# Kernel optimization log

Measured on AMD Instinct MI355X. Metric: run time of the kernel, lower is better.

## Reference

```python
import jax, jax.numpy as jnp
import numpy as np

RES = 0.1
TABLE = 1 << 20  # hash_table_size, power of two
PRIMES = np.array([73856093, 19349669, 83492791], dtype=np.int64)
FEAT_DIM = 120
BMIN = (-2.6, -8.1, 0.0)
BMAX = (4.6, 4.7, 3.1)
M_QUERIES = 1_000_000
CORNERS = np.array([[0,0,0],[1,0,0],[0,1,0],[0,0,1],[1,1,0],[1,0,1],[0,1,1],[1,1,1]], dtype=np.int32)


def _build_table():
    # Replicates build_hash_grid(): first-come voxel index per hash slot, collisions skipped.
    xs = np.arange(BMIN[0], BMAX[0], RES, dtype=np.float32)
    ys = np.arange(BMIN[1], BMAX[1], RES, dtype=np.float32)
    zs = np.arange(BMIN[2], BMAX[2], RES, dtype=np.float32)
    gx, gy, gz = np.meshgrid(xs, ys, zs, indexing='ij')
    coords = np.stack([gx, gy, gz], -1).reshape(-1, 3)
    gc = np.floor(coords / RES).astype(np.int64)
    h = np.remainder((gc * PRIMES).sum(-1), TABLE)
    n = coords.shape[0]
    buf = np.full(TABLE, -1, dtype=np.int32)
    buf[h[::-1]] = np.arange(n, dtype=np.int32)[::-1]
    return buf, n


def setup_inputs() -> dict:
    key = jax.random.key(0)
    k1, k2 = jax.random.split(key)
    buf, n_vox = _build_table()
    lo = jnp.array(BMIN, jnp.float32)
    hi = jnp.array(BMAX, jnp.float32)
    query_pts = lo + (hi - lo) * jax.random.uniform(k1, (M_QUERIES, 3), dtype=jnp.float32)
    features = 0.01 * jax.random.normal(k2, (n_vox, FEAT_DIM), dtype=jnp.float32)
    return {
        "query_pts": query_pts,
        "features": features,
        "buffer_voxel_index": jnp.asarray(buf),  # int32 [TABLE]
    }


def reference(query_pts, features, buffer_voxel_index):
    """query_voxel_feature with trilinear_feat=True: 8-corner hash lookup + trilinear blend."""
    primes_u = jnp.asarray(PRIMES.astype(np.uint32))
    gcf = query_pts / RES                        # [M,3]
    floor = jnp.floor(gcf)
    frac = gcf - floor                           # [M,3]
    base = floor.astype(jnp.int32)               # [M,3]
    acc = jnp.zeros((query_pts.shape[0], features.shape[1]), dtype=features.dtype)
    for c in CORNERS:                            # fixed 8-iteration corner loop
        cj = jnp.asarray(c)
        cc = base + cj                           # [M,3]
        # TABLE is a power of two, so low-20-bits of wrapping uint32 arithmetic
        # equals the exact int64 remainder used by torch.
        h = ((cc.astype(jnp.uint32) * primes_u).sum(-1) & (TABLE - 1)).astype(jnp.int32)
        vidx = buffer_voxel_index[h]             # [M], -1 for empty slots
        w = jnp.where(cj == 0, 1.0 - frac, frac).prod(-1)  # [M] trilinear weight
        w = jnp.where(vidx >= 0, w, 0.0)
        acc = acc + features[jnp.maximum(vidx, 0)] * w[:, None]
    return acc
```

## Files before the change

### kernel.cpp

```cpp
#include <hip/hip_runtime.h>


#define TABLE_MASK ((1u << 20) - 1u)
#define FEAT_DIM 120
#define ROW_STRIDE 120
#define NROWS 75
#define NCHUNK 30
#define TOTCH (NROWS * NCHUNK)
#define NSLOT 5
#define NXCD 8
#define C8 32

#define NBINS_X 32
#define NBINS_Y 64
#define NBINS_Z 16
#define NBINS (NBINS_X * NBINS_Y * NBINS_Z)

typedef float f4 __attribute__((ext_vector_type(4)));

__global__ __launch_bounds__(256) void zero_kernel(int* __restrict__ hist8) {
    const int i = blockIdx.x * blockDim.x + threadIdx.x;
    if (i < NXCD * NBINS + 2) hist8[i] = 0;
}

__global__ __launch_bounds__(256) void bin_kernel(
    const float* __restrict__ qp, int* __restrict__ hist8,
    f4* __restrict__ sq8, f4* __restrict__ ovf, int Cr, int M)
{
    const int q = blockIdx.x * blockDim.x + threadIdx.x;
    if (q >= M) return;

    int xcd;
    asm volatile("s_getreg_b32 %0, hwreg(HW_REG_XCC_ID)" : "=s"(xcd));
    xcd &= (NXCD - 1);

    const float gx = qp[3 * q + 0] / 0.1f;
    const float gy = qp[3 * q + 1] / 0.1f;
    const float gz = qp[3 * q + 2] / 0.1f;
    const int bx = (int)floorf(gx);
    const int by = (int)floorf(gy);
    const int bz = (int)floorf(gz);
    const int kx = ((bx + 32) >> 2) & (NBINS_X - 1);
    const int ky = ((by + 96) >> 2) & (NBINS_Y - 1);
    const int kz = (bz >> 1) & (NBINS_Z - 1);
    const int key = ((kx * NBINS_Y) + ky) * NBINS_Z + kz;

    const int pos = __hip_atomic_fetch_add(&hist8[xcd * NBINS + key], 1,
                                           __ATOMIC_RELAXED,
                                           __HIP_MEMORY_SCOPE_WORKGROUP);
    f4 s;
    s.x = gx; s.y = gy; s.z = gz; s.w = __int_as_float(q);
    if (pos < Cr) {
        sq8[((size_t)xcd * NBINS + key) * C8 + pos] = s;
    } else {
        const int o = atomicAdd(&hist8[NXCD * NBINS], 1);
        if (o < M) ovf[o] = s;
    }
}

__global__ __launch_bounds__(256) void compact_kernel(
    const int* __restrict__ hist8, int* __restrict__ nact,
    int* __restrict__ list)
{
    const int i = blockIdx.x * blockDim.x + threadIdx.x;
    if (i >= NBINS) return;
    int tot = 0;
#pragma unroll
    for (int s = 0; s < NXCD; ++s) tot += hist8[s * NBINS + i];
    if (tot > 0) {
        const int p = atomicAdd(nact, 1);
        list[p] = i;
    }
}

__global__ __launch_bounds__(512, 4) void voxel_trilinear_kernel(
    const f4*    __restrict__ sq8,
    const float* __restrict__ feat,
    const int*   __restrict__ table,
    const int*   __restrict__ hist8,
    const int*   __restrict__ nactp,
    const int*   __restrict__ list,
    float*       __restrict__ out,
    int Cr)
{
    __shared__ f4    sqL[NXCD * C8];
    __shared__ float rows[NROWS * ROW_STRIDE];

    const int t = threadIdx.x;
    const int nact = *nactp;
    const int stride = gridDim.x;

    if (blockIdx.x >= nact) return;

    f4   rreg[NSLOT];
    f4   qreg;
    bool qok = false;
    int  qdst = 0;
    int  total = 0;

    auto prefetch = [&](int wg) {
        int c[8];
#pragma unroll
        for (int i = 0; i < 8; ++i) {
            int v = hist8[i * NBINS + wg];
            c[i] = (v > Cr) ? Cr : v;
        }
        total = 0;
#pragma unroll
        for (int i = 0; i < 8; ++i) total += c[i];

        qok = false;
        if (t < 256) {
            const int seg = t >> 5, lane = t & 31;
            int p = 0;
#pragma unroll
            for (int i = 0; i < 8; ++i) p += (i < seg) ? c[i] : 0;
            if (lane < c[seg]) {
                qok = true;
                qdst = p + lane;
                qreg = sq8[((size_t)seg * NBINS + wg) * C8 + lane];
            }
        }

        const int binx = wg >> 10;
        const int biny = (wg >> 4) & 63;
        const int binz = wg & 15;
        const int vx0 = binx * 4 - 32;
        const int vy0 = biny * 4 - 96;
        const int vz0 = binz * 2;
#pragma unroll
        for (int s = 0; s < NSLOT; ++s) {
            const int idx = t + s * 512;
            f4 val = (f4)(0.0f);
            if (idx < TOTCH) {
                const int row = idx / NCHUNK;
                const int chunk = idx - row * NCHUNK;
                const int i = row / 15;
                const int j = (row / 3) % 5;
                const int k = row % 3;
                const unsigned h = (unsigned)(vx0 + i) * 73856093u
                                 + (unsigned)(vy0 + j) * 19349669u
                                 + (unsigned)(vz0 + k) * 83492791u;
                const int v = table[h & TABLE_MASK];
                if (v >= 0)
                    val = *reinterpret_cast<const f4*>(
                        feat + (size_t)v * FEAT_DIM + chunk * 4);
            }
            rreg[s] = val;
        }
    };

    prefetch(list[blockIdx.x]);

    for (int bi = blockIdx.x; bi < nact; bi += stride) {
        __syncthreads();

#pragma unroll
        for (int s = 0; s < NSLOT; ++s) {
            const int idx = t + s * 512;
            if (idx < TOTCH)
                *reinterpret_cast<f4*>(rows + idx * 4) = rreg[s];
        }
        if (qok) sqL[qdst] = qreg;
        const int ct = total;
        __syncthreads();

        const int nb = bi + stride;
        if (nb < nact) prefetch(list[nb]);

        const int group = t >> 4;
        const int l = t & 15;
        const int CX[8] = {0, 1, 0, 0, 1, 1, 0, 1};
        const int CY[8] = {0, 0, 1, 0, 1, 0, 1, 1};
        const int CZ[8] = {0, 0, 0, 1, 0, 1, 1, 1};

        for (int qs = group; qs < ct; qs += 32) {
            const f4 qv = sqL[qs];
            const float rx = qv.x - floorf(qv.x);
            const float ry = qv.y - floorf(qv.y);
            const float rz = qv.z - floorf(qv.z);
            const int q = __float_as_int(qv.w);
            const int lx = ((int)floorf(qv.x) + 32) & 3;
            const int ly = ((int)floorf(qv.y) + 96) & 3;
            const int lz = (int)floorf(qv.z) & 1;

            const float sx = 1.0f - rx, sy = 1.0f - ry, sz = 1.0f - rz;
            float w[8];
            w[0] = sx * sy * sz;
            w[1] = rx * sy * sz;
            w[2] = sx * ry * sz;
            w[3] = sx * sy * rz;
            w[4] = rx * ry * sz;
            w[5] = rx * sy * rz;
            w[6] = sx * ry * rz;
            w[7] = rx * ry * rz;

            f4 a0 = (f4)(0.0f), a1 = (f4)(0.0f);
#pragma unroll
            for (int k = 0; k < 8; ++k) {
                const int row = ((lx + CX[k]) * 5 + (ly + CY[k])) * 3 + (lz + CZ[k]);
                const float* rp = rows + row * ROW_STRIDE;
                const f4 fa = *reinterpret_cast<const f4*>(rp + l * 4);
                const f4 fb = *reinterpret_cast<const f4*>(rp + 56 + l * 4);
                a0 += fa * w[k];
                a1 += fb * w[k];
            }

            float* po = out + (size_t)q * FEAT_DIM;
            __builtin_nontemporal_store(a0, reinterpret_cast<f4*>(po + l * 4));
            if (l >= 2)
                __builtin_nontemporal_store(a1, reinterpret_cast<f4*>(po + 56 + l * 4));
        }
    }
}

__global__ __launch_bounds__(256) void ovf_kernel(
    const f4*    __restrict__ ovf,
    const int*   __restrict__ hist8,
    const float* __restrict__ feat,
    const int*   __restrict__ table,
    float*       __restrict__ out,
    int M)
{
    int n = hist8[NXCD * NBINS];
    if (n > M) n = M;
    if (n == 0) return;

    const int nthreads = gridDim.x * 256;
    for (int i = blockIdx.x * 256 + threadIdx.x; i < n * 16; i += nthreads) {
        const int g = i >> 4;
        const int l = i & 15;
        const f4 qv = ovf[g];
        const float gx = qv.x, gy = qv.y, gz = qv.z;
        const int q = __float_as_int(qv.w);
        const float flx = floorf(gx), fly = floorf(gy), flz = floorf(gz);
        const float rx = gx - flx, ry = gy - fly, rz = gz - flz;
        const int bx = (int)flx, by = (int)fly, bz = (int)flz;

        const unsigned hx0 = (unsigned)bx * 73856093u;
        const unsigned hy0 = (unsigned)by * 19349669u;
        const unsigned hz0 = (unsigned)bz * 83492791u;
        const unsigned hx1 = hx0 + 73856093u;
        const unsigned hy1 = hy0 + 19349669u;
        const unsigned hz1 = hz0 + 83492791u;

        unsigned h[8];
        h[0] = (hx0 + hy0 + hz0) & TABLE_MASK;
        h[1] = (hx1 + hy0 + hz0) & TABLE_MASK;
        h[2] = (hx0 + hy1 + hz0) & TABLE_MASK;
        h[3] = (hx0 + hy0 + hz1) & TABLE_MASK;
        h[4] = (hx1 + hy1 + hz0) & TABLE_MASK;
        h[5] = (hx1 + hy0 + hz1) & TABLE_MASK;
        h[6] = (hx0 + hy1 + hz1) & TABLE_MASK;
        h[7] = (hx1 + hy1 + hz1) & TABLE_MASK;

        int vidx[8];
#pragma unroll
        for (int k = 0; k < 8; ++k) vidx[k] = table[h[k]];

        const float sxw = 1.0f - rx, syw = 1.0f - ry, szw = 1.0f - rz;
        float w[8];
        w[0] = sxw * syw * szw;
        w[1] = rx  * syw * szw;
        w[2] = sxw * ry  * szw;
        w[3] = sxw * syw * rz;
        w[4] = rx  * ry  * szw;
        w[5] = rx  * syw * rz;
        w[6] = sxw * ry  * rz;
        w[7] = rx  * ry  * rz;

        f4 a0 = (f4)(0.0f), a1 = (f4)(0.0f);
#pragma unroll
        for (int k = 0; k < 8; ++k) {
            const int v = vidx[k] >= 0 ? vidx[k] : 0;
            const float wk = vidx[k] >= 0 ? w[k] : 0.0f;
            const float* rp = feat + (size_t)v * FEAT_DIM;
            const f4 fa = *reinterpret_cast<const f4*>(rp + l * 4);
            const f4 fb = *reinterpret_cast<const f4*>(rp + 56 + l * 4);
            a0 += fa * wk;
            a1 += fb * wk;
        }

        float* po = out + (size_t)q * FEAT_DIM;
        __builtin_nontemporal_store(a0, reinterpret_cast<f4*>(po + l * 4));
        if (l >= 2)
            __builtin_nontemporal_store(a1, reinterpret_cast<f4*>(po + 56 + l * 4));
    }
}

extern "C" void kernel_launch(void* const* d_in, const int* in_sizes, int n_in,
                              void* d_out, int out_size, void* d_ws, size_t ws_size,
                              hipStream_t stream) {
    const float* qp    = (const float*)d_in[0];
    const float* feat  = (const float*)d_in[1];
    const int*   table = (const int*)d_in[2];
    float*       out   = (float*)d_out;

    const int M = in_sizes[0] / 3;

    const size_t histB = ((NXCD * NBINS + 2) * sizeof(int) + 15) & ~(size_t)15;
    const size_t listB = (NBINS * sizeof(int) + 15) & ~(size_t)15;
    int* hist8 = (int*)d_ws;
    int* nact  = hist8 + NXCD * NBINS + 1;
    int* list  = (int*)((char*)d_ws + histB);
    f4*  ovf   = (f4*)((char*)d_ws + histB + listB);
    f4*  sq8   = ovf + M;

    const size_t fixed = histB + listB + (size_t)M * 16;
    size_t cap = (ws_size > fixed)
               ? (ws_size - fixed) / ((size_t)NXCD * NBINS * 16) : 0;
    int Cr = (cap > C8) ? C8 : (int)cap;
    if (Cr < 1) Cr = 1;

    const int block = 256;
    zero_kernel<<<(NXCD * NBINS + 2 + block - 1) / block, block, 0, stream>>>(hist8);
    bin_kernel<<<(M + block - 1) / block, block, 0, stream>>>(qp, hist8, sq8, ovf, Cr, M);
    compact_kernel<<<(NBINS + block - 1) / block, block, 0, stream>>>(hist8, nact, list);
    voxel_trilinear_kernel<<<1024, 512, 0, stream>>>(sq8, feat, table, hist8,
                                                     nact, list, out, Cr);
    ovf_kernel<<<512, 256, 0, stream>>>(ovf, hist8, feat, table, out, M);
}
```

Baseline: 234.5 us.

## Order bins big-first and shrink per-XCD slot capacity to twelve

Compaction now splits active bins into a big list (at least 40 points) filled from the front and a small list filled from the back, so the persistent voxel kernel processes heavy bins first and light edge bins last. The per-XCD slot capacity per bin is reduced from 32 to 12, shrinking the staging buffer and the threads used to load queries into shared memory. Points beyond the capacity spill to the slower overflow kernel, so more queries may take the global per-point path.

```diff
diff --git a/kernel.cpp b/kernel.cpp
--- a/kernel.cpp
+++ b/kernel.cpp
@@ -9,7 +9,8 @@
 #define TOTCH (NROWS * NCHUNK)
 #define NSLOT 5
 #define NXCD 8
-#define C8 32
+#define C8 12
+#define BIGTHR 40
 
 #define NBINS_X 32
 #define NBINS_Y 64
@@ -20,7 +21,7 @@
 
 __global__ __launch_bounds__(256) void zero_kernel(int* __restrict__ hist8) {
     const int i = blockIdx.x * blockDim.x + threadIdx.x;
-    if (i < NXCD * NBINS + 2) hist8[i] = 0;
+    if (i < NXCD * NBINS + 3) hist8[i] = 0;
 }
 
 __global__ __launch_bounds__(256) void bin_kernel(
@@ -59,17 +60,18 @@
 }
 
 __global__ __launch_bounds__(256) void compact_kernel(
-    const int* __restrict__ hist8, int* __restrict__ nact,
-    int* __restrict__ list)
+    const int* __restrict__ hist8, int* __restrict__ nbig,
+    int* __restrict__ nsmall, int* __restrict__ list)
 {
     const int i = blockIdx.x * blockDim.x + threadIdx.x;
     if (i >= NBINS) return;
     int tot = 0;
 #pragma unroll
     for (int s = 0; s < NXCD; ++s) tot += hist8[s * NBINS + i];
-    if (tot > 0) {
-        const int p = atomicAdd(nact, 1);
-        list[p] = i;
+    if (tot >= BIGTHR) {
+        list[atomicAdd(nbig, 1)] = i;
+    } else if (tot > 0) {
+        list[NBINS - 1 - atomicAdd(nsmall, 1)] = i;
     }
 }
 
@@ -78,7 +80,8 @@
     const float* __restrict__ feat,
     const int*   __restrict__ table,
     const int*   __restrict__ hist8,
-    const int*   __restrict__ nactp,
+    const int*   __restrict__ nbigp,
+    const int*   __restrict__ nsmallp,
     const int*   __restrict__ list,
     float*       __restrict__ out,
     int Cr)
@@ -87,10 +90,15 @@
     __shared__ float rows[NROWS * ROW_STRIDE];
 
     const int t = threadIdx.x;
-    const int nact = *nactp;
+    const int nbig = *nbigp;
+    const int nact = nbig + *nsmallp;
     const int stride = gridDim.x;
 
     if (blockIdx.x >= nact) return;
+
+    auto binat = [&](int i) {
+        return list[(i < nbig) ? i : (NBINS - 1 - (i - nbig))];
+    };
 
     f4   rreg[NSLOT];
     f4   qreg;
@@ -110,8 +118,8 @@
         for (int i = 0; i < 8; ++i) total += c[i];
 
         qok = false;
-        if (t < 256) {
-            const int seg = t >> 5, lane = t & 31;
+        if (t < 128) {
+            const int seg = t >> 4, lane = t & 15;
             int p = 0;
 #pragma unroll
             for (int i = 0; i < 8; ++i) p += (i < seg) ? c[i] : 0;
@@ -150,7 +158,7 @@
         }
     };
 
-    prefetch(list[blockIdx.x]);
+    prefetch(binat(blockIdx.x));
 
     for (int bi = blockIdx.x; bi < nact; bi += stride) {
         __syncthreads();
@@ -166,7 +174,7 @@
         __syncthreads();
 
         const int nb = bi + stride;
-        if (nb < nact) prefetch(list[nb]);
+        if (nb < nact) prefetch(binat(nb));
 
         const int group = t >> 4;
         const int l = t & 15;
@@ -298,13 +306,14 @@
 
     const int M = in_sizes[0] / 3;
 
-    const size_t histB = ((NXCD * NBINS + 2) * sizeof(int) + 15) & ~(size_t)15;
+    const size_t histB = ((NXCD * NBINS + 3) * sizeof(int) + 15) & ~(size_t)15;
     const size_t listB = (NBINS * sizeof(int) + 15) & ~(size_t)15;
-    int* hist8 = (int*)d_ws;
-    int* nact  = hist8 + NXCD * NBINS + 1;
-    int* list  = (int*)((char*)d_ws + histB);
-    f4*  ovf   = (f4*)((char*)d_ws + histB + listB);
-    f4*  sq8   = ovf + M;
+    int* hist8  = (int*)d_ws;
+    int* nbig   = hist8 + NXCD * NBINS + 1;
+    int* nsmall = hist8 + NXCD * NBINS + 2;
+    int* list   = (int*)((char*)d_ws + histB);
+    f4*  ovf    = (f4*)((char*)d_ws + histB + listB);
+    f4*  sq8    = ovf + M;
 
     const size_t fixed = histB + listB + (size_t)M * 16;
     size_t cap = (ws_size > fixed)
@@ -313,10 +322,10 @@
     if (Cr < 1) Cr = 1;
 
     const int block = 256;
-    zero_kernel<<<(NXCD * NBINS + 2 + block - 1) / block, block, 0, stream>>>(hist8);
+    zero_kernel<<<(NXCD * NBINS + 3 + block - 1) / block, block, 0, stream>>>(hist8);
     bin_kernel<<<(M + block - 1) / block, block, 0, stream>>>(qp, hist8, sq8, ovf, Cr, M);
-    compact_kernel<<<(NBINS + block - 1) / block, block, 0, stream>>>(hist8, nact, list);
+    compact_kernel<<<(NBINS + block - 1) / block, block, 0, stream>>>(hist8, nbig, nsmall, list);
     voxel_trilinear_kernel<<<1024, 512, 0, stream>>>(sq8, feat, table, hist8,
-                                                     nact, list, out, Cr);
+                                                     nbig, nsmall, list, out, Cr);
     ovf_kernel<<<512, 256, 0, stream>>>(ovf, hist8, feat, table, out, M);
 }
```

Measured after the change: 453.7 us. +93.4%, slower.
